# Kernel optimization log

Hardware: AMD Instinct MI355X
Metric: run time of the kernel (lower is better)

## Reference

```python
import jax, jax.numpy as jnp
import numpy as np

# Layered-DAG regularization of the dynamic active_path graph.
H, N, BATCH, D, R = 6, 16, 32, 512, 64   # hop levels, nodes/level, batch, dim, low-rank
M = (H - 1) * N                           # nodes with weights (levels 1..H-1)
ETA_W = 0.015
LAM_C, LAM_R = 0.65, 0.35
THETA0 = 0.5
SPEC_MIN, SPEC_MAX = 0.3, 4.0
BETA1, BETA2, EPS = 0.9, 0.999, 1e-8
W_MAX = float(np.sqrt(D) * 2.0)
DW_CLIP = 5.0


def _spectral_norm(A1, B1):
    # largest singular value of W = A1 @ B1.T via power iteration using only low-rank products
    d = A1.shape[0]
    def body(_, u):
        w = A1 @ (B1.T @ (B1 @ (A1.T @ u)))  # (W W^T) u
        return w / (jnp.linalg.norm(w) + 1e-12)
    u0 = jnp.ones((d,), A1.dtype) / jnp.sqrt(jnp.asarray(d, A1.dtype))
    u = jax.lax.fori_loop(0, 20, body, u0)
    return jnp.linalg.norm(B1 @ (A1.T @ u))


def _update_node(A1, B1, mA, vA, mB, vB, Vin, T_local):
    # dual-signal (contrastive + retrograde) weight update, Adam step t=1, is_positive=True
    W = A1 @ B1.T                       # (D, D)
    Vw = Vin @ W.T                      # (BATCH, D) pre-activation (record.V_weighted)
    Vout = jnp.tanh(Vw)                 # record.V_out (tanh primitive)
    fprime = 1.0 - Vout ** 2            # primitive_derivative for tanh
    goodness = (Vout ** 2).sum(-1).mean()
    theta = THETA0 * ((Vin ** 2).sum(-1).mean() + 1e-9)   # goodness_scale_input=True
    delta = goodness - theta
    Vout_grad = (Vout * fprime * delta).mean(0)
    Vin_mean = Vin.mean(0)
    dW_c = jnp.outer(Vout_grad, Vin_mean)
    dW_r = jnp.outer(T_local.mean(0) * fprime.mean(0), Vin_mean)
    dW = LAM_C * dW_c + LAM_R * dW_r
    gnorm = jnp.linalg.norm(dW)
    dW = dW * jnp.where(gnorm > DW_CLIP, DW_CLIP / (gnorm + 1e-12), 1.0)
    gA = dW @ B1
    gB = dW.T @ A1
    mA_n = BETA1 * mA + (1 - BETA1) * gA
    vA_n = BETA2 * vA + (1 - BETA2) * gA ** 2
    A_new = A1 - ETA_W * (mA_n / (1 - BETA1)) / (jnp.sqrt(vA_n / (1 - BETA2)) + EPS)
    mB_n = BETA1 * mB + (1 - BETA1) * gB
    vB_n = BETA2 * vB + (1 - BETA2) * gB ** 2
    B_new = B1 - ETA_W * (mB_n / (1 - BETA1)) / (jnp.sqrt(vB_n / (1 - BETA2)) + EPS)
    return jnp.clip(A_new, -W_MAX, W_MAX), jnp.clip(B_new, -W_MAX, W_MAX)


def _forward(Y_hat, Y_star, V_edges, A, Bw, m_A, v_A, m_B, v_B):
    T_v = (Y_star - Y_hat) / jnp.sqrt(jnp.asarray(D, Y_hat.dtype))
    mse = jnp.mean((Y_star - Y_hat) ** 2)

    # proportional blame: per-edge mean-over-batch L2 norm of the contribution
    norms = jnp.linalg.norm(V_edges, axis=-1).mean(-1)           # (H-1, Ndst, Nsrc)
    w_blame = norms / (norms.sum(-1, keepdims=True) + 1e-9)

    spec = jax.vmap(jax.vmap(_spectral_norm))(A, Bw)             # (H-1, N)
    scale = jax.lax.stop_gradient(jnp.clip(spec, SPEC_MIN, SPEC_MAX))  # torch.tensor() detaches

    # retrograde flow in reverse topological (hop) order; output node = (level H-1, node 0)
    T_top = jnp.zeros((N, BATCH, D), Y_hat.dtype).at[0].set(T_v)

    def step(T_curr, xs):
        w_h, s_h = xs                                            # (Ndst,Nsrc), (Ndst,)
        tnorm = jnp.linalg.norm(T_curr, axis=-1).mean(-1)        # (Ndst,)
        edge_t = s_h[:, None] * w_h * tnorm[:, None]             # ||T_upstream|| per edge
        T_prev = jnp.einsum('j,ji,jbd->ibd', s_h, w_h, T_curr)   # blame-weighted scatter
        return T_prev, (T_prev, edge_t)

    _, (Ts, edge_t) = jax.lax.scan(step, T_top, (w_blame[::-1], scale[::-1]))
    T_all = jnp.concatenate([Ts[::-1], T_top[None]], axis=0)     # (H, N, BATCH, D), by level
    edge_tensions = edge_t[::-1]                                 # (H-1, Ndst, Nsrc)

    V_in = V_edges.sum(axis=2)                                   # inbox sum -> (H-1, N, BATCH, D)
    T_upd = T_all[1:]                                            # tensions at non-input nodes

    sh = (M, D, R)
    A_new, B_new = jax.vmap(_update_node)(
        A.reshape(sh), Bw.reshape(sh), m_A.reshape(sh), v_A.reshape(sh),
        m_B.reshape(sh), v_B.reshape(sh),
        V_in.reshape(M, BATCH, D), T_upd.reshape(M, BATCH, D))
    return (mse, edge_tensions,
            A_new.reshape(H - 1, N, D, R), B_new.reshape(H - 1, N, D, R), T_all)


def setup_inputs():
    key = jax.random.key(0)
    k = jax.random.split(key, 7)
    sd = 1.0 / np.sqrt(D)
    return {
        "Y_hat": jax.random.normal(k[0], (BATCH, D), jnp.float32),
        "Y_star": jax.random.normal(k[1], (BATCH, D), jnp.float32),
        "V_edges": jax.random.normal(k[2], (H - 1, N, N, BATCH, D), jnp.float32),
        "A": jax.random.normal(k[3], (H - 1, N, D, R), jnp.float32) * sd,
        "Bw": jax.random.normal(k[4], (H - 1, N, D, R), jnp.float32) * sd,
        "m_A": jnp.zeros((H - 1, N, D, R), jnp.float32),
        "v_A": jax.random.uniform(k[5], (H - 1, N, D, R), jnp.float32) * 1e-4,
        "m_B": jnp.zeros((H - 1, N, D, R), jnp.float32),
        "v_B": jax.random.uniform(k[6], (H - 1, N, D, R), jnp.float32) * 1e-4,
    }


def reference(Y_hat, Y_star, V_edges, A, Bw, m_A, v_A, m_B, v_B):
    return _forward(Y_hat, Y_star, V_edges, A, Bw, m_A, v_A, m_B, v_B)
```

## Files before the change

### kernel.cpp

```cpp
#include <hip/hip_runtime.h>
#include <math.h>

#define DEV static __device__ __forceinline__

constexpr int NB    = 16;
constexpr int BATCH = 32;
constexpr int DDIM  = 512;
constexpr int RK    = 64;
constexpr int LAY   = 5;
constexpr int MM    = 80;
constexpr int TLS   = NB * BATCH * DDIM;

constexpr float ETA_W   = 0.015f;
constexpr float LAM_C   = 0.65f, LAM_R = 0.35f;
constexpr float THETA0  = 0.5f;
constexpr float SPEC_MIN = 0.3f, SPEC_MAX = 4.0f;
constexpr float DW_CLIP = 5.0f;
constexpr float W_MAX   = 45.254833995939045f;
constexpr float RSQ_D   = 0.044194173824159216f;

constexpr int OUT_MSE  = 0;
constexpr int OUT_EDGE = 1;
constexpr int OUT_A    = 1281;
constexpr int OUT_B    = OUT_A + MM * DDIM * RK;
constexpr int OUT_T    = OUT_B + MM * DDIM * RK;

constexpr int SCR_GP   = 1284;
constexpr int SCR_YV   = 2622724;
constexpr int SCR_VIN  = 5244164;

constexpr int WS_NORMB  = 0;
constexpr int WS_TVN    = 40960;
constexpr int WS_TVM    = 41000;
constexpr int WS_COEF   = 41600;
constexpr int WS_SCALE  = 41700;
constexpr int WS_Y0P    = 41800;
constexpr int WS_VM     = 62300;
constexpr int WS_P      = 103300;
constexpr int WS_Q      = 108450;
constexpr int WS_GC     = 113600;

DEV float wave_reduce(float v) {
  #pragma unroll
  for (int o = 32; o > 0; o >>= 1) v += __shfl_down(v, o, 64);
  return v;
}

DEV float block_reduce_512(float v, float* sred) {
  v = wave_reduce(v);
  __syncthreads();
  if ((threadIdx.x & 63) == 0) sred[threadIdx.x >> 6] = v;
  __syncthreads();
  float s = 0.f;
  #pragma unroll
  for (int k = 0; k < 8; ++k) s += sred[k];
  return s;
}

DEV float bcast_lane(float v, int lane) {
  return __int_as_float(__builtin_amdgcn_readlane(__float_as_int(v), lane));
}

__global__ __launch_bounds__(256) void k_stage1(const float* __restrict__ V,
    const float* __restrict__ yh, const float* __restrict__ ys,
    const float* __restrict__ Aw, const float* __restrict__ Bww,
    float* __restrict__ out, float* __restrict__ ws) {
  __shared__ float smem[8448];
  int bid = blockIdx.x, t = threadIdx.x;
  if (bid < 2560) {
    float* nbuf = smem;
    float* vbuf = smem + 2048;
    int b = bid & 31, j = (bid >> 5) & 15, hh = bid >> 9;
    const float* base = V + (size_t)(((hh*16 + j)*16)*32 + b) * 512;
    int g = t >> 7, u = t & 127;
    float vx = 0.f, vy = 0.f, vz = 0.f, vw = 0.f;
    #pragma unroll
    for (int io = 0; io < 8; ++io) {
      int i = io * 2 + g;
      float4 v = ((const float4*)(base + (size_t)i * 16384))[u];
      nbuf[i * 128 + u] = v.x*v.x + v.y*v.y + v.z*v.z + v.w*v.w;
      vx += v.x; vy += v.y; vz += v.z; vw += v.w;
    }
    vbuf[g * 512 + u * 4 + 0] = vx;
    vbuf[g * 512 + u * 4 + 1] = vy;
    vbuf[g * 512 + u * 4 + 2] = vz;
    vbuf[g * 512 + u * 4 + 3] = vw;
    __syncthreads();
    {
      float2 o;
      o.x = vbuf[2 * t]     + vbuf[512 + 2 * t];
      o.y = vbuf[2 * t + 1] + vbuf[512 + 2 * t + 1];
      ((float2*)(out + SCR_VIN + (size_t)((hh*16 + j)*32 + b) * 512))[t] = o;
    }
    int w = t >> 6, lane = t & 63;
    #pragma unroll
    for (int k = 0; k < 4; ++k) {
      int i = w * 4 + k;
      float s = nbuf[i * 128 + lane] + nbuf[i * 128 + lane + 64];
      s = wave_reduce(s);
      if (lane == 0)
        ws[WS_NORMB + (size_t)b * 1280 + (hh*16 + j) * 16 + i] = sqrtf(s);
    }
  } else if (bid < 2592) {
    int b = bid - 2560;
    float2 a = ((const float2*)(yh + (size_t)b * 512))[t];
    float2 c = ((const float2*)(ys + (size_t)b * 512))[t];
    float d0 = c.x - a.x, d1 = c.y - a.y;
    float s = d0*d0 + d1*d1;
    s = wave_reduce(s);
    if ((t & 63) == 0) smem[t >> 6] = s;
    __syncthreads();
    if (t == 0)
      ws[WS_TVN + b] = sqrtf(smem[0]+smem[1]+smem[2]+smem[3]) * RSQ_D;
  } else if (bid == 2592) {
    float s = 0.f;
    for (int i = t; i < 4096; i += 256) {
      float4 a = ((const float4*)yh)[i], b = ((const float4*)ys)[i];
      float d0 = b.x-a.x, d1 = b.y-a.y, d2 = b.z-a.z, d3 = b.w-a.w;
      s += d0*d0 + d1*d1 + d2*d2 + d3*d3;
    }
    s = wave_reduce(s);
    if ((t & 63) == 0) smem[t >> 6] = s;
    __syncthreads();
    if (t == 0)
      out[OUT_MSE] = (smem[0]+smem[1]+smem[2]+smem[3]) * (1.f/16384.f);
  } else if (bid == 2593) {
    float s0 = 0.f, s1 = 0.f;
    #pragma unroll 4
    for (int b = 0; b < 32; ++b) {
      s0 += ys[b*512 + t]       - yh[b*512 + t];
      s1 += ys[b*512 + t + 256] - yh[b*512 + t + 256];
    }
    ws[WS_TVM + t]       = s0 * (RSQ_D / 32.f);
    ws[WS_TVM + t + 256] = s1 * (RSQ_D / 32.f);
  } else {
    float* tile = smem;
    float (*y0s)[64] = (float(*)[64])(smem + 8192);
    int bid0 = bid - 2594;
    int slice = bid0 & 3, side = (bid0 >> 2) & 1, m = bid0 >> 3;
    const float* src = (side ? Bww : Aw) + (size_t)m * 32768 + slice * 8192;
    #pragma unroll
    for (int k = 0; k < 8; ++k)
      ((float4*)tile)[t + k * 256] = ((const float4*)src)[t + k * 256];
    __syncthreads();
    {
      int r = t & 63, q = t >> 6;
      float s = 0.f;
      #pragma unroll 8
      for (int dd = q * 32; dd < q * 32 + 32; ++dd) s += tile[dd * 64 + r];
      y0s[q][r] = s;
    }
    __syncthreads();
    if (side == 0 && t < 64)
      ws[WS_Y0P + (m * 4 + slice) * 64 + t] = y0s[0][t] + y0s[1][t] + y0s[2][t] + y0s[3][t];
    float acc[4][4];
    #pragma unroll
    for (int i = 0; i < 4; ++i)
      #pragma unroll
      for (int k = 0; k < 4; ++k) acc[i][k] = 0.f;
    int r1 = (t >> 4) * 4, r2 = (t & 15) * 4;
    #pragma unroll 4
    for (int dd = 0; dd < 128; ++dd) {
      float4 a1 = *(const float4*)&tile[dd * 64 + r1];
      float4 a2 = *(const float4*)&tile[dd * 64 + r2];
      float av[4] = {a1.x, a1.y, a1.z, a1.w};
      float bv[4] = {a2.x, a2.y, a2.z, a2.w};
      #pragma unroll
      for (int i = 0; i < 4; ++i)
        #pragma unroll
        for (int k = 0; k < 4; ++k) acc[i][k] += av[i] * bv[k];
    }
    float* outp = out + SCR_GP + (size_t)((m * 2 + side) * 4 + slice) * 4096;
    #pragma unroll
    for (int i = 0; i < 4; ++i) {
      float4 v; v.x = acc[i][0]; v.y = acc[i][1]; v.z = acc[i][2]; v.w = acc[i][3];
      *(float4*)&outp[(r1 + i) * 64 + r2] = v;
    }
  }
}

__global__ __launch_bounds__(256, 1) void k_pyv(const float* __restrict__ Bww,
    float* __restrict__ out, float* __restrict__ ws) {
  int bid = blockIdx.x, t = threadIdx.x;
  if (bid < 80) {
    if (t >= 64) return;
    int m = bid;
    int r = t;
    const float* gp = out + SCR_GP + (size_t)(m * 2 + 0) * 16384;
    const float* hp = out + SCR_GP + (size_t)(m * 2 + 1) * 16384;
    float Gc[64], Hc[64];
    #pragma unroll
    for (int c4 = 0; c4 < 16; ++c4) {
      const float* gb = gp + r * 64 + c4 * 4;
      float4 g0 = *(const float4*)(gb);
      float4 g1 = *(const float4*)(gb + 4096);
      float4 g2 = *(const float4*)(gb + 8192);
      float4 g3 = *(const float4*)(gb + 12288);
      Gc[c4*4+0] = g0.x+g1.x+g2.x+g3.x;
      Gc[c4*4+1] = g0.y+g1.y+g2.y+g3.y;
      Gc[c4*4+2] = g0.z+g1.z+g2.z+g3.z;
      Gc[c4*4+3] = g0.w+g1.w+g2.w+g3.w;
      const float* hb = hp + r * 64 + c4 * 4;
      float4 h0 = *(const float4*)(hb);
      float4 h1 = *(const float4*)(hb + 4096);
      float4 h2 = *(const float4*)(hb + 8192);
      float4 h3 = *(const float4*)(hb + 12288);
      Hc[c4*4+0] = h0.x+h1.x+h2.x+h3.x;
      Hc[c4*4+1] = h0.y+h1.y+h2.y+h3.y;
      Hc[c4*4+2] = h0.z+h1.z+h2.z+h3.z;
      Hc[c4*4+3] = h0.w+h1.w+h2.w+h3.w;
    }
    float y = (ws[WS_Y0P + (m*4+0)*64 + r] + ws[WS_Y0P + (m*4+1)*64 + r] +
               ws[WS_Y0P + (m*4+2)*64 + r] + ws[WS_Y0P + (m*4+3)*64 + r]) * RSQ_D;
    for (int it = 0; it < 20; ++it) {
      float z0 = 0.f, z1 = 0.f, z2 = 0.f, z3 = 0.f;
      #pragma unroll
      for (int c = 0; c < 16; ++c) {
        z0 = fmaf(Hc[c],      bcast_lane(y, c),      z0);
        z1 = fmaf(Hc[c + 16], bcast_lane(y, c + 16), z1);
        z2 = fmaf(Hc[c + 32], bcast_lane(y, c + 32), z2);
        z3 = fmaf(Hc[c + 48], bcast_lane(y, c + 48), z3);
      }
      float z = (z0 + z1) + (z2 + z3);
      float t0 = 0.f, t1 = 0.f, t2 = 0.f, t3 = 0.f;
      #pragma unroll
      for (int c = 0; c < 16; ++c) {
        t0 = fmaf(Gc[c],      bcast_lane(z, c),      t0);
        t1 = fmaf(Gc[c + 16], bcast_lane(z, c + 16), t1);
        t2 = fmaf(Gc[c + 32], bcast_lane(z, c + 32), t2);
        t3 = fmaf(Gc[c + 48], bcast_lane(z, c + 48), t3);
      }
      float tt = (t0 + t1) + (t2 + t3);
      float zt = z * tt;
      #pragma unroll
      for (int o = 32; o > 0; o >>= 1) zt += __shfl_xor(zt, o, 64);
      y = tt / (sqrtf(zt) + 1e-12f);
    }
    float z0 = 0.f, z1 = 0.f, z2 = 0.f, z3 = 0.f;
    #pragma unroll
    for (int c = 0; c < 16; ++c) {
      z0 = fmaf(Hc[c],      bcast_lane(y, c),      z0);
      z1 = fmaf(Hc[c + 16], bcast_lane(y, c + 16), z1);
      z2 = fmaf(Hc[c + 32], bcast_lane(y, c + 32), z2);
      z3 = fmaf(Hc[c + 48], bcast_lane(y, c + 48), z3);
    }
    float z = (z0 + z1) + (z2 + z3);
    float yz = y * z;
    #pragma unroll
    for (int o = 32; o > 0; o >>= 1) yz += __shfl_xor(yz, o, 64);
    if (r == 0)
      ws[WS_SCALE + m] = fminf(fmaxf(sqrtf(yz), SPEC_MIN), SPEC_MAX);
  } else {
    int bid0 = bid - 80;
    int m = bid0 >> 1, half = bid0 & 1;
    int w = t >> 6, r = t & 63;
    int b0 = half * 16 + w * 4;
    const float* Bm = Bww + (size_t)m * 32768;
    const float* Vm = out + SCR_VIN + (size_t)m * 16384;
    float acc0 = 0.f, acc1 = 0.f, acc2 = 0.f, acc3 = 0.f;
    #pragma unroll 2
    for (int d = 0; d < 512; d += 4) {
      float br0 = Bm[(d+0)*64 + r];
      float br1 = Bm[(d+1)*64 + r];
      float br2 = Bm[(d+2)*64 + r];
      float br3 = Bm[(d+3)*64 + r];
      float4 v0 = *(const float4*)(Vm + (b0+0)*512 + d);
      float4 v1 = *(const float4*)(Vm + (b0+1)*512 + d);
      float4 v2 = *(const float4*)(Vm + (b0+2)*512 + d);
      float4 v3 = *(const float4*)(Vm + (b0+3)*512 + d);
      acc0 += br0*v0.x + br1*v0.y + br2*v0.z + br3*v0.w;
      acc1 += br0*v1.x + br1*v1.y + br2*v1.z + br3*v1.w;
      acc2 += br0*v2.x + br1*v2.y + br2*v2.z + br3*v2.w;
      acc3 += br0*v3.x + br1*v3.y + br2*v3.z + br3*v3.w;
    }
    float* Yv = out + SCR_YV + (size_t)m * 2048;
    Yv[(b0+0)*64 + r] = acc0;
    Yv[(b0+1)*64 + r] = acc1;
    Yv[(b0+2)*64 + r] = acc2;
    Yv[(b0+3)*64 + r] = acc3;
  }
}

__global__ __launch_bounds__(512) void k_vw(const float* __restrict__ Aw,
    float* __restrict__ out, float* __restrict__ ws) {
  __shared__ float ubuf[2176];
  __shared__ float gcol[512];
  __shared__ float sred[8];
  __shared__ float coefs[96];
  int m = blockIdx.x;
  int t = threadIdx.x;
  int hh = m >> 4, j = m & 15;
  const float* A1  = Aw + (size_t)m * 32768;
  const float* Vin = out + SCR_VIN + (size_t)m * 16384;
  const float* YvG = out + SCR_YV + (size_t)m * 2048;

  if (t < 256) {
    #pragma unroll
    for (int h = 0; h < 5; ++h) {
      float n = 0.f;
      #pragma unroll 8
      for (int b = 0; b < 32; ++b)
        n += ws[WS_NORMB + (size_t)b * 1280 + h * 256 + t];
      n *= (1.f / 32.f);
      float s = n;
      s += __shfl_xor(s, 1, 64);
      s += __shfl_xor(s, 2, 64);
      s += __shfl_xor(s, 4, 64);
      s += __shfl_xor(s, 8, 64);
      ubuf[h * 256 + t] = ws[WS_SCALE + h * 16 + (t >> 4)] * n / (s + 1e-9f);
    }
    if (t < 16) coefs[80 + t] = (t == 0) ? 1.f : 0.f;
  }
  __syncthreads();
  if (t < 16) {
    for (int h = 4; h >= 0; --h) {
      float s = 0.f;
      #pragma unroll
      for (int jj = 0; jj < 16; ++jj)
        s += ubuf[h * 256 + jj * 16 + t] * coefs[(h + 1) * 16 + jj];
      coefs[h * 16 + t] = s;
    }
  }
  __syncthreads();
  if (m == 0) {
    if (t < 256) {
      float tvs = 0.f;
      #pragma unroll
      for (int b = 0; b < 32; ++b) tvs += ws[WS_TVN + b];
      float tvmean = tvs * (1.f / 32.f);
      #pragma unroll
      for (int h = 0; h < 5; ++h)
        out[OUT_EDGE + h * 256 + t] = ubuf[h * 256 + t] * coefs[(h + 1) * 16 + (t >> 4)] * tvmean;
    }
    if (t < 96) ws[WS_COEF + t] = coefs[t];
  }
  float coefval = coefs[(hh + 1) * 16 + j];
  __syncthreads();

  {
    int b = t >> 4, r0 = (t & 15) * 4;
    float4 y4 = *(const float4*)(YvG + t * 4);
    *(float4*)&ubuf[b * 68 + r0] = y4;
  }
  __syncthreads();
  if (t < 64) {
    float s = 0.f;
    #pragma unroll 8
    for (int b = 0; b < 32; ++b) s += ubuf[b * 68 + t];
    ws[WS_P + m * 64 + t] = s * (1.f / 32.f);
  }
  int d = t;
  float ar[64];
  #pragma unroll
  for (int k = 0; k < 16; ++k)
    *(float4*)&ar[k * 4] = *(const float4*)(A1 + d * 64 + k * 4);
  float tmean, ssin, ssvm;
  {
    float sv = 0.f, sq = 0.f;
    #pragma unroll 4
    for (int b = 0; b < 32; ++b) {
      float v = Vin[b * 512 + d];
      sv += v; sq += v * v;
    }
    float vmean = sv * (1.f / 32.f);
    tmean = coefval * ws[WS_TVM + d];
    ws[WS_VM + m * 512 + d] = vmean;
    ssin = block_reduce_512(sq, sred) * (1.f / 32.f);
    ssvm = block_reduce_512(vmean * vmean, sred);
  }
  float gs = 0.f, vga = 0.f, fpa = 0.f;
  for (int b = 0; b < 32; ++b) {
    const float* yb = &ubuf[b * 68];
    float a0 = 0.f, a1 = 0.f, a2 = 0.f, a3 = 0.f;
    #pragma unroll
    for (int k = 0; k < 4; ++k) {
      float4 y0 = *(const float4*)&yb[k * 16 + 0];
      float4 y1 = *(const float4*)&yb[k * 16 + 4];
      float4 y2 = *(const float4*)&yb[k * 16 + 8];
      float4 y3 = *(const float4*)&yb[k * 16 + 12];
      a0 += ar[k*16+ 0]*y0.x + ar[k*16+ 1]*y0.y + ar[k*16+ 2]*y0.z + ar[k*16+ 3]*y0.w;
      a1 += ar[k*16+ 4]*y1.x + ar[k*16+ 5]*y1.y + ar[k*16+ 6]*y1.z + ar[k*16+ 7]*y1.w;
      a2 += ar[k*16+ 8]*y2.x + ar[k*16+ 9]*y2.y + ar[k*16+10]*y2.z + ar[k*16+11]*y2.w;
      a3 += ar[k*16+12]*y3.x + ar[k*16+13]*y3.y + ar[k*16+14]*y3.z + ar[k*16+15]*y3.w;
    }
    float vw = (a0 + a1) + (a2 + a3);
    float x = fminf(fmaxf(vw * 2.f, -40.f), 40.f);
    float e = __expf(x);
    float vo = (e - 1.f) / (e + 1.f);
    float fp = 1.f - vo * vo;
    gs  += vo * vo;
    vga += vo * fp;
    fpa += fp;
  }
  float goodness = block_reduce_512(gs, sred) * (1.f / 32.f);
  float delta = goodness - THETA0 * (ssin + 1e-9f);
  {
    float g = LAM_C * delta * vga * (1.f / 32.f) + LAM_R * tmean * (fpa * (1.f / 32.f));
    float gn2 = block_reduce_512(g * g, sred);
    float gnorm = sqrtf(gn2) * sqrtf(ssvm);
    float clipf = gnorm > DW_CLIP ? DW_CLIP / (gnorm + 1e-12f) : 1.f;
    float gcv = g * clipf;
    ws[WS_GC + m * 512 + d] = gcv;
    gcol[d] = gcv;
  }
  __syncthreads();
  {
    int r = t & 63, dq = t >> 6;
    float s = 0.f;
    #pragma unroll 4
    for (int k = 0; k < 64; ++k) {
      int dd = dq * 64 + k;
      s += gcol[dd] * A1[dd * 64 + r];
    }
    ubuf[dq * 64 + r] = s;
  }
  __syncthreads();
  if (t < 64) {
    float s = 0.f;
    #pragma unroll
    for (int p8 = 0; p8 < 8; ++p8) s += ubuf[p8 * 64 + t];
    ws[WS_Q + m * 64 + t] = s;
  }
}

constexpr int TW_BLOCKS = 1536;
constexpr int AD_HALF4  = 655360;

__global__ __launch_bounds__(256) void k_final(const float* __restrict__ yh,
    const float* __restrict__ ys,
    const float* __restrict__ Aw, const float* __restrict__ Bww,
    const float* __restrict__ mA, const float* __restrict__ vA,
    const float* __restrict__ mB, const float* __restrict__ vB,
    const float* __restrict__ ws, float* __restrict__ out) {
  int bid = blockIdx.x, t = threadIdx.x;
  if (bid < TW_BLOCKS) {
    int g0 = (bid * 256 + t) * 4;
    int li = g0 >> 14;
    int bd = g0 & 16383;
    float4 a = *(const float4*)(yh + bd);
    float4 b = *(const float4*)(ys + bd);
    float cf = ws[WS_COEF + li] * RSQ_D;
    out[OUT_T + g0 + 0] = cf * (b.x - a.x);
    out[OUT_T + g0 + 1] = cf * (b.y - a.y);
    out[OUT_T + g0 + 2] = cf * (b.z - a.z);
    out[OUT_T + g0 + 3] = cf * (b.w - a.w);
    return;
  }
  int idx = (bid - TW_BLOCKS) * 256 + t;
  bool isB = idx >= AD_HALF4;
  int e = (isB ? idx - AD_HALF4 : idx) * 4;
  int m = e >> 15;
  int rem = e & 32767;
  int d = rem >> 6;
  int r = rem & 63;
  float4 g4;
  const float *w0, *m0, *v0;
  int obase;
  if (!isB) {
    float gc = ws[WS_GC + m * 512 + d];
    float4 p = *(const float4*)&ws[WS_P + m * 64 + r];
    g4.x = gc * p.x; g4.y = gc * p.y; g4.z = gc * p.z; g4.w = gc * p.w;
    w0 = Aw; m0 = mA; v0 = vA; obase = OUT_A;
  } else {
    float vm = ws[WS_VM + m * 512 + d];
    float4 q = *(const float4*)&ws[WS_Q + m * 64 + r];
    g4.x = vm * q.x; g4.y = vm * q.y; g4.z = vm * q.z; g4.w = vm * q.w;
    w0 = Bww; m0 = mB; v0 = vB; obase = OUT_B;
  }
  float4 a4 = *(const float4*)&w0[e];
  float4 mm4 = *(const float4*)&m0[e];
  float4 vv4 = *(const float4*)&v0[e];
  float ga[4] = {g4.x, g4.y, g4.z, g4.w};
  float aa[4] = {a4.x, a4.y, a4.z, a4.w};
  float ma[4] = {mm4.x, mm4.y, mm4.z, mm4.w};
  float va[4] = {vv4.x, vv4.y, vv4.z, vv4.w};
  #pragma unroll
  for (int i = 0; i < 4; ++i) {
    float g = ga[i];
    float mn = 0.9f * ma[i] + 0.1f * g;
    float vn = 0.999f * va[i] + 0.001f * g * g;
    float u = aa[i] - ETA_W * (mn * 10.f) / (sqrtf(vn * 1000.f) + 1e-8f);
    u = fminf(fmaxf(u, -W_MAX), W_MAX);
    out[obase + e + i] = u;
  }
}

extern "C" void kernel_launch(void* const* d_in, const int* in_sizes, int n_in,
                              void* d_out, int out_size, void* d_ws, size_t ws_size,
                              hipStream_t stream) {
  (void)in_sizes; (void)n_in; (void)out_size; (void)ws_size;
  const float* Yh = (const float*)d_in[0];
  const float* Ys = (const float*)d_in[1];
  const float* V  = (const float*)d_in[2];
  const float* Aw = (const float*)d_in[3];
  const float* Bw = (const float*)d_in[4];
  const float* mA = (const float*)d_in[5];
  const float* vA = (const float*)d_in[6];
  const float* mB = (const float*)d_in[7];
  const float* vB = (const float*)d_in[8];
  float* out = (float*)d_out;
  float* ws  = (float*)d_ws;

  k_stage1<<<2594 + 640, 256, 0, stream>>>(V, Yh, Ys, Aw, Bw, out, ws);
  k_pyv<<<240, 256, 0, stream>>>(Bw, out, ws);
  k_vw<<<80, 512, 0, stream>>>(Aw, out, ws);
  k_final<<<TW_BLOCKS + 2 * (AD_HALF4 / 256), 256, 0, stream>>>(
      Yh, Ys, Aw, Bw, mA, vA, mB, vB, ws, out);
}
```

Before: 115.5 us.

## Halve k_stage1 shared tile and shrink k_vw to 256 threads with two columns each

The Gram-matrix branch of k_stage1 now loads its 128-row slice in two 64-row halves through a 4096-float tile, accumulating the column sums across halves. This halves the static shared memory of every k_stage1 block, including the V-reduction blocks, so more blocks can be resident per CU. k_vw drops from 512 to 256 threads per block, with each thread handling two d columns (two 64-float A rows held in registers) and block reductions reduced to 4 waves. The gain in occupancy and fewer sync partners is traded for an extra barrier round in k_stage1 and doubled register pressure in k_vw, which could cause spills.

```diff
diff --git a/kernel.cpp b/kernel.cpp
--- a/kernel.cpp
+++ b/kernel.cpp
@@ -46,15 +46,12 @@
   return v;
 }
 
-DEV float block_reduce_512(float v, float* sred) {
+DEV float block_reduce_256(float v, float* sred) {
   v = wave_reduce(v);
   __syncthreads();
   if ((threadIdx.x & 63) == 0) sred[threadIdx.x >> 6] = v;
   __syncthreads();
-  float s = 0.f;
-  #pragma unroll
-  for (int k = 0; k < 8; ++k) s += sred[k];
-  return s;
+  return sred[0] + sred[1] + sred[2] + sred[3];
 }
 
 DEV float bcast_lane(float v, int lane) {
@@ -65,7 +62,7 @@
     const float* __restrict__ yh, const float* __restrict__ ys,
     const float* __restrict__ Aw, const float* __restrict__ Bww,
     float* __restrict__ out, float* __restrict__ ws) {
-  __shared__ float smem[8448];
+  __shared__ float smem[4352];
   int bid = blockIdx.x, t = threadIdx.x;
   if (bid < 2560) {
     float* nbuf = smem;
@@ -135,41 +132,47 @@
     ws[WS_TVM + t + 256] = s1 * (RSQ_D / 32.f);
   } else {
     float* tile = smem;
-    float (*y0s)[64] = (float(*)[64])(smem + 8192);
+    float (*y0s)[64] = (float(*)[64])(smem + 4096);
     int bid0 = bid - 2594;
     int slice = bid0 & 3, side = (bid0 >> 2) & 1, m = bid0 >> 3;
     const float* src = (side ? Bww : Aw) + (size_t)m * 32768 + slice * 8192;
-    #pragma unroll
-    for (int k = 0; k < 8; ++k)
-      ((float4*)tile)[t + k * 256] = ((const float4*)src)[t + k * 256];
-    __syncthreads();
-    {
-      int r = t & 63, q = t >> 6;
-      float s = 0.f;
-      #pragma unroll 8
-      for (int dd = q * 32; dd < q * 32 + 32; ++dd) s += tile[dd * 64 + r];
-      y0s[q][r] = s;
-    }
-    __syncthreads();
-    if (side == 0 && t < 64)
-      ws[WS_Y0P + (m * 4 + slice) * 64 + t] = y0s[0][t] + y0s[1][t] + y0s[2][t] + y0s[3][t];
     float acc[4][4];
     #pragma unroll
     for (int i = 0; i < 4; ++i)
       #pragma unroll
       for (int k = 0; k < 4; ++k) acc[i][k] = 0.f;
+    float y0acc = 0.f;
     int r1 = (t >> 4) * 4, r2 = (t & 15) * 4;
-    #pragma unroll 4
-    for (int dd = 0; dd < 128; ++dd) {
-      float4 a1 = *(const float4*)&tile[dd * 64 + r1];
-      float4 a2 = *(const float4*)&tile[dd * 64 + r2];
-      float av[4] = {a1.x, a1.y, a1.z, a1.w};
-      float bv[4] = {a2.x, a2.y, a2.z, a2.w};
+    for (int half = 0; half < 2; ++half) {
+      __syncthreads();
       #pragma unroll
-      for (int i = 0; i < 4; ++i)
+      for (int k = 0; k < 4; ++k)
+        ((float4*)tile)[t + k * 256] = ((const float4*)(src + half * 4096))[t + k * 256];
+      __syncthreads();
+      {
+        int r = t & 63, q = t >> 6;
+        float s = 0.f;
+        #pragma unroll 8
+        for (int dd = q * 16; dd < q * 16 + 16; ++dd) s += tile[dd * 64 + r];
+        y0s[q][r] = s;
+      }
+      __syncthreads();
+      if (side == 0 && t < 64)
+        y0acc += y0s[0][t] + y0s[1][t] + y0s[2][t] + y0s[3][t];
+      #pragma unroll 4
+      for (int dd = 0; dd < 64; ++dd) {
+        float4 a1 = *(const float4*)&tile[dd * 64 + r1];
+        float4 a2 = *(const float4*)&tile[dd * 64 + r2];
+        float av[4] = {a1.x, a1.y, a1.z, a1.w};
+        float bv[4] = {a2.x, a2.y, a2.z, a2.w};
         #pragma unroll
-        for (int k = 0; k < 4; ++k) acc[i][k] += av[i] * bv[k];
-    }
+        for (int i = 0; i < 4; ++i)
+          #pragma unroll
+          for (int k = 0; k < 4; ++k) acc[i][k] += av[i] * bv[k];
+      }
+    }
+    if (side == 0 && t < 64)
+      ws[WS_Y0P + (m * 4 + slice) * 64 + t] = y0acc;
     float* outp = out + SCR_GP + (size_t)((m * 2 + side) * 4 + slice) * 4096;
     #pragma unroll
     for (int i = 0; i < 4; ++i) {
@@ -281,11 +284,11 @@
   }
 }
 
-__global__ __launch_bounds__(512) void k_vw(const float* __restrict__ Aw,
+__global__ __launch_bounds__(256) void k_vw(const float* __restrict__ Aw,
     float* __restrict__ out, float* __restrict__ ws) {
   __shared__ float ubuf[2176];
   __shared__ float gcol[512];
-  __shared__ float sred[8];
+  __shared__ float sred[4];
   __shared__ float coefs[96];
   int m = blockIdx.x;
   int t = threadIdx.x;
@@ -294,23 +297,21 @@
   const float* Vin = out + SCR_VIN + (size_t)m * 16384;
   const float* YvG = out + SCR_YV + (size_t)m * 2048;
 
-  if (t < 256) {
-    #pragma unroll
-    for (int h = 0; h < 5; ++h) {
-      float n = 0.f;
-      #pragma unroll 8
-      for (int b = 0; b < 32; ++b)
-        n += ws[WS_NORMB + (size_t)b * 1280 + h * 256 + t];
-      n *= (1.f / 32.f);
-      float s = n;
-      s += __shfl_xor(s, 1, 64);
-      s += __shfl_xor(s, 2, 64);
-      s += __shfl_xor(s, 4, 64);
-      s += __shfl_xor(s, 8, 64);
-      ubuf[h * 256 + t] = ws[WS_SCALE + h * 16 + (t >> 4)] * n / (s + 1e-9f);
-    }
-    if (t < 16) coefs[80 + t] = (t == 0) ? 1.f : 0.f;
-  }
+  #pragma unroll
+  for (int h = 0; h < 5; ++h) {
+    float n = 0.f;
+    #pragma unroll 8
+    for (int b = 0; b < 32; ++b)
+      n += ws[WS_NORMB + (size_t)b * 1280 + h * 256 + t];
+    n *= (1.f / 32.f);
+    float s = n;
+    s += __shfl_xor(s, 1, 64);
+    s += __shfl_xor(s, 2, 64);
+    s += __shfl_xor(s, 4, 64);
+    s += __shfl_xor(s, 8, 64);
+    ubuf[h * 256 + t] = ws[WS_SCALE + h * 16 + (t >> 4)] * n / (s + 1e-9f);
+  }
+  if (t < 16) coefs[80 + t] = (t == 0) ? 1.f : 0.f;
   __syncthreads();
   if (t < 16) {
     for (int h = 4; h >= 0; --h) {
@@ -323,23 +324,22 @@
   }
   __syncthreads();
   if (m == 0) {
-    if (t < 256) {
-      float tvs = 0.f;
-      #pragma unroll
-      for (int b = 0; b < 32; ++b) tvs += ws[WS_TVN + b];
-      float tvmean = tvs * (1.f / 32.f);
-      #pragma unroll
-      for (int h = 0; h < 5; ++h)
-        out[OUT_EDGE + h * 256 + t] = ubuf[h * 256 + t] * coefs[(h + 1) * 16 + (t >> 4)] * tvmean;
-    }
+    float tvs = 0.f;
+    #pragma unroll
+    for (int b = 0; b < 32; ++b) tvs += ws[WS_TVN + b];
+    float tvmean = tvs * (1.f / 32.f);
+    #pragma unroll
+    for (int h = 0; h < 5; ++h)
+      out[OUT_EDGE + h * 256 + t] = ubuf[h * 256 + t] * coefs[(h + 1) * 16 + (t >> 4)] * tvmean;
     if (t < 96) ws[WS_COEF + t] = coefs[t];
   }
   float coefval = coefs[(hh + 1) * 16 + j];
   __syncthreads();
 
-  {
-    int b = t >> 4, r0 = (t & 15) * 4;
-    float4 y4 = *(const float4*)(YvG + t * 4);
+  #pragma unroll
+  for (int u = t; u < 512; u += 256) {
+    int b = u >> 4, r0 = (u & 15) * 4;
+    float4 y4 = *(const float4*)(YvG + u * 4);
     *(float4*)&ubuf[b * 68 + r0] = y4;
   }
   __syncthreads();
@@ -349,67 +349,84 @@
     for (int b = 0; b < 32; ++b) s += ubuf[b * 68 + t];
     ws[WS_P + m * 64 + t] = s * (1.f / 32.f);
   }
-  int d = t;
-  float ar[64];
+  int d0 = t, d1 = t + 256;
+  float ar0[64], ar1[64];
   #pragma unroll
-  for (int k = 0; k < 16; ++k)
-    *(float4*)&ar[k * 4] = *(const float4*)(A1 + d * 64 + k * 4);
-  float tmean, ssin, ssvm;
+  for (int k = 0; k < 16; ++k) {
+    *(float4*)&ar0[k * 4] = *(const float4*)(A1 + d0 * 64 + k * 4);
+    *(float4*)&ar1[k * 4] = *(const float4*)(A1 + d1 * 64 + k * 4);
+  }
+  float tmean0, tmean1, ssin, ssvm;
   {
-    float sv = 0.f, sq = 0.f;
+    float sv0 = 0.f, sq0 = 0.f, sv1 = 0.f, sq1 = 0.f;
     #pragma unroll 4
     for (int b = 0; b < 32; ++b) {
-      float v = Vin[b * 512 + d];
-      sv += v; sq += v * v;
-    }
-    float vmean = sv * (1.f / 32.f);
-    tmean = coefval * ws[WS_TVM + d];
-    ws[WS_VM + m * 512 + d] = vmean;
-    ssin = block_reduce_512(sq, sred) * (1.f / 32.f);
-    ssvm = block_reduce_512(vmean * vmean, sred);
-  }
-  float gs = 0.f, vga = 0.f, fpa = 0.f;
+      float v0 = Vin[b * 512 + d0];
+      float v1 = Vin[b * 512 + d1];
+      sv0 += v0; sq0 += v0 * v0;
+      sv1 += v1; sq1 += v1 * v1;
+    }
+    float vm0 = sv0 * (1.f / 32.f), vm1 = sv1 * (1.f / 32.f);
+    tmean0 = coefval * ws[WS_TVM + d0];
+    tmean1 = coefval * ws[WS_TVM + d1];
+    ws[WS_VM + m * 512 + d0] = vm0;
+    ws[WS_VM + m * 512 + d1] = vm1;
+    ssin = block_reduce_256(sq0 + sq1, sred) * (1.f / 32.f);
+    ssvm = block_reduce_256(vm0 * vm0 + vm1 * vm1, sred);
+  }
+  float gs = 0.f, vga0 = 0.f, fpa0 = 0.f, vga1 = 0.f, fpa1 = 0.f;
   for (int b = 0; b < 32; ++b) {
     const float* yb = &ubuf[b * 68];
-    float a0 = 0.f, a1 = 0.f, a2 = 0.f, a3 = 0.f;
+    float p00 = 0.f, p01 = 0.f, p10 = 0.f, p11 = 0.f;
     #pragma unroll
     for (int k = 0; k < 4; ++k) {
       float4 y0 = *(const float4*)&yb[k * 16 + 0];
       float4 y1 = *(const float4*)&yb[k * 16 + 4];
       float4 y2 = *(const float4*)&yb[k * 16 + 8];
       float4 y3 = *(const float4*)&yb[k * 16 + 12];
-      a0 += ar[k*16+ 0]*y0.x + ar[k*16+ 1]*y0.y + ar[k*16+ 2]*y0.z + ar[k*16+ 3]*y0.w;
-      a1 += ar[k*16+ 4]*y1.x + ar[k*16+ 5]*y1.y + ar[k*16+ 6]*y1.z + ar[k*16+ 7]*y1.w;
-      a2 += ar[k*16+ 8]*y2.x + ar[k*16+ 9]*y2.y + ar[k*16+10]*y2.z + ar[k*16+11]*y2.w;
-      a3 += ar[k*16+12]*y3.x + ar[k*16+13]*y3.y + ar[k*16+14]*y3.z + ar[k*16+15]*y3.w;
-    }
-    float vw = (a0 + a1) + (a2 + a3);
-    float x = fminf(fmaxf(vw * 2.f, -40.f), 40.f);
-    float e = __expf(x);
-    float vo = (e - 1.f) / (e + 1.f);
-    float fp = 1.f - vo * vo;
-    gs  += vo * vo;
-    vga += vo * fp;
-    fpa += fp;
-  }
-  float goodness = block_reduce_512(gs, sred) * (1.f / 32.f);
+      p00 += ar0[k*16+ 0]*y0.x + ar0[k*16+ 1]*y0.y + ar0[k*16+ 2]*y0.z + ar0[k*16+ 3]*y0.w
+           + ar0[k*16+ 4]*y1.x + ar0[k*16+ 5]*y1.y + ar0[k*16+ 6]*y1.z + ar0[k*16+ 7]*y1.w;
+      p01 += ar0[k*16+ 8]*y2.x + ar0[k*16+ 9]*y2.y + ar0[k*16+10]*y2.z + ar0[k*16+11]*y2.w
+           + ar0[k*16+12]*y3.x + ar0[k*16+13]*y3.y + ar0[k*16+14]*y3.z + ar0[k*16+15]*y3.w;
+      p10 += ar1[k*16+ 0]*y0.x + ar1[k*16+ 1]*y0.y + ar1[k*16+ 2]*y0.z + ar1[k*16+ 3]*y0.w
+           + ar1[k*16+ 4]*y1.x + ar1[k*16+ 5]*y1.y + ar1[k*16+ 6]*y1.z + ar1[k*16+ 7]*y1.w;
+      p11 += ar1[k*16+ 8]*y2.x + ar1[k*16+ 9]*y2.y + ar1[k*16+10]*y2.z + ar1[k*16+11]*y2.w
+           + ar1[k*16+12]*y3.x + ar1[k*16+13]*y3.y + ar1[k*16+14]*y3.z + ar1[k*16+15]*y3.w;
+    }
+    float vw0 = p00 + p01;
+    float vw1 = p10 + p11;
+    float x0 = fminf(fmaxf(vw0 * 2.f, -40.f), 40.f);
+    float e0 = __expf(x0);
+    float vo0 = (e0 - 1.f) / (e0 + 1.f);
+    float fp0 = 1.f - vo0 * vo0;
+    gs += vo0 * vo0; vga0 += vo0 * fp0; fpa0 += fp0;
+    float x1 = fminf(fmaxf(vw1 * 2.f, -40.f), 40.f);
+    float e1 = __expf(x1);
+    float vo1 = (e1 - 1.f) / (e1 + 1.f);
+    float fp1 = 1.f - vo1 * vo1;
+    gs += vo1 * vo1; vga1 += vo1 * fp1; fpa1 += fp1;
+  }
+  float goodness = block_reduce_256(gs, sred) * (1.f / 32.f);
   float delta = goodness - THETA0 * (ssin + 1e-9f);
   {
-    float g = LAM_C * delta * vga * (1.f / 32.f) + LAM_R * tmean * (fpa * (1.f / 32.f));
-    float gn2 = block_reduce_512(g * g, sred);
+    float g0 = LAM_C * delta * vga0 * (1.f / 32.f) + LAM_R * tmean0 * (fpa0 * (1.f / 32.f));
+    float g1 = LAM_C * delta * vga1 * (1.f / 32.f) + LAM_R * tmean1 * (fpa1 * (1.f / 32.f));
+    float gn2 = block_reduce_256(g0 * g0 + g1 * g1, sred);
     float gnorm = sqrtf(gn2) * sqrtf(ssvm);
     float clipf = gnorm > DW_CLIP ? DW_CLIP / (gnorm + 1e-12f) : 1.f;
-    float gcv = g * clipf;
-    ws[WS_GC + m * 512 + d] = gcv;
-    gcol[d] = gcv;
+    float gcv0 = g0 * clipf, gcv1 = g1 * clipf;
+    ws[WS_GC + m * 512 + d0] = gcv0;
+    ws[WS_GC + m * 512 + d1] = gcv1;
+    gcol[d0] = gcv0;
+    gcol[d1] = gcv1;
   }
   __syncthreads();
   {
     int r = t & 63, dq = t >> 6;
     float s = 0.f;
     #pragma unroll 4
-    for (int k = 0; k < 64; ++k) {
-      int dd = dq * 64 + k;
+    for (int k = 0; k < 128; ++k) {
+      int dd = dq * 128 + k;
       s += gcol[dd] * A1[dd * 64 + r];
     }
     ubuf[dq * 64 + r] = s;
@@ -418,7 +435,7 @@
   if (t < 64) {
     float s = 0.f;
     #pragma unroll
-    for (int p8 = 0; p8 < 8; ++p8) s += ubuf[p8 * 64 + t];
+    for (int p4 = 0; p4 < 4; ++p4) s += ubuf[p4 * 64 + t];
     ws[WS_Q + m * 64 + t] = s;
   }
 }
@@ -503,7 +520,7 @@
 
   k_stage1<<<2594 + 640, 256, 0, stream>>>(V, Yh, Ys, Aw, Bw, out, ws);
   k_pyv<<<240, 256, 0, stream>>>(Bw, out, ws);
-  k_vw<<<80, 512, 0, stream>>>(Aw, out, ws);
+  k_vw<<<80, 256, 0, stream>>>(Aw, out, ws);
   k_final<<<TW_BLOCKS + 2 * (AD_HALF4 / 256), 256, 0, stream>>>(
       Yh, Ys, Aw, Bw, mA, vA, mB, vB, ws, out);
 }
```

After: 117.1 us. About the same (+1.4%).
